# Kernel optimization log

Measured on AMD Instinct MI355X. Metric: run time of the kernel, lower is better.

The kernel has to match this reference:

```python
import jax, jax.numpy as jnp
import numpy as np

B, S, D = 4, 2048, 1024
NEG = -1.0e9


def setup_inputs() -> dict:
    key = jax.random.key(0)
    kq, kk, kv = jax.random.split(key, 3)
    query = jax.random.normal(kq, (B, S, D), dtype=jnp.float32)
    k = jax.random.normal(kk, (B, S, D), dtype=jnp.float32)
    value = jax.random.normal(kv, (B, S, D), dtype=jnp.float32)
    # causal mask: tril(ones(S,S)) with leading broadcast dim, as in the source script
    mask = jnp.tril(jnp.ones((S, S), dtype=jnp.int32))[None, :, :]
    return {"query": query, "key": k, "value": value, "mask": mask}


def reference(query, key, value, mask):
    d_q = query.shape[-1]
    scale = 1.0 / jnp.sqrt(jnp.float32(d_q))
    # [B, S, S] score matrix
    scores = jnp.einsum("bqd,bkd->bqk", query, key) * scale
    scores = jnp.where(mask == 0, jnp.float32(NEG), scores)
    attn = jax.nn.softmax(scores, axis=-1)
    out = jnp.einsum("bqk,bkd->bqd", attn, value)
    return (out, attn)
```

## Files before the change

kernel.cpp:

```cpp
#include <hip/hip_runtime.h>

#define Bn 4
#define Sn 2048
#define Dn 1024

typedef short bf16x8 __attribute__((ext_vector_type(8)));
typedef float f32x4 __attribute__((ext_vector_type(4)));

__device__ __forceinline__ unsigned f2bf(float x) {
    unsigned u = __float_as_uint(x);
    return (u + 0x7FFFu + ((u >> 16) & 1u)) >> 16;
}

__device__ __forceinline__ uint2 pack4(float4 v) {
    uint2 p;
    p.x = f2bf(v.x) | (f2bf(v.y) << 16);
    p.y = f2bf(v.z) | (f2bf(v.w) << 16);
    return p;
}

__device__ __forceinline__ float bf2f(unsigned short s) {
    return __uint_as_float((unsigned)s << 16);
}

__device__ __forceinline__ void gl_lds16(const unsigned short* g, unsigned short* l) {
    __builtin_amdgcn_global_load_lds(
        (const __attribute__((address_space(1))) unsigned int*)g,
        (__attribute__((address_space(3))) unsigned int*)l, 16, 0, 0);
}

__global__ __launch_bounds__(256) void convert_qk_kernel(
    const float* __restrict__ Q, const float* __restrict__ K,
    unsigned short* __restrict__ Q16, unsigned short* __restrict__ K16) {
    size_t i = (size_t)blockIdx.x * 256 + threadIdx.x;
    float4 q = ((const float4*)Q)[i];
    ((uint2*)Q16)[i] = pack4(q);
    float4 k = ((const float4*)K)[i];
    ((uint2*)K16)[i] = pack4(k);
}

__global__ __launch_bounds__(256) void transpose_v_kernel(
    const float* __restrict__ V, unsigned short* __restrict__ Vt) {
    __shared__ unsigned short Ts[128 * 66];
    const int s0 = blockIdx.x * 128, d0 = blockIdx.y * 64, b = blockIdx.z;
    const float* Vb = V + ((size_t)b * Sn + s0) * Dn + d0;
    const int t = threadIdx.x;
#pragma unroll
    for (int i = 0; i < 8; i++) {
        int task = i * 256 + t;
        int r = task >> 4, c4 = task & 15;
        float4 v = *(const float4*)(Vb + (size_t)r * Dn + c4 * 4);
        *(uint2*)(&Ts[r * 66 + c4 * 4]) = pack4(v);
    }
    __syncthreads();
    unsigned short* Vtb = Vt + ((size_t)b * Dn + d0) * Sn + s0;
#pragma unroll
    for (int i = 0; i < 4; i++) {
        int task = i * 256 + t;
        int sc = task & 15, dr = task >> 4;
        unsigned short tmp[8];
#pragma unroll
        for (int j = 0; j < 8; j++) tmp[j] = Ts[(sc * 8 + j) * 66 + dr];
        uint4 u;
        u.x = tmp[0] | ((unsigned)tmp[1] << 16);
        u.y = tmp[2] | ((unsigned)tmp[3] << 16);
        u.z = tmp[4] | ((unsigned)tmp[5] << 16);
        u.w = tmp[6] | ((unsigned)tmp[7] << 16);
        *(uint4*)(&Vtb[(size_t)dr * Sn + sc * 8]) = u;
    }
}

__global__ __launch_bounds__(256) void qk_scores_kernel(
    const unsigned short* __restrict__ Q16, const unsigned short* __restrict__ K16,
    unsigned short* __restrict__ S16) {
    const int wid = blockIdx.x;
    int qt = (int)((sqrtf(8.0f * wid + 1.0f) - 1.0f) * 0.5f);
    while (qt * (qt + 1) / 2 > wid) qt--;
    while ((qt + 1) * (qt + 2) / 2 <= wid) qt++;
    const int kt = wid - qt * (qt + 1) / 2;
    const int b = blockIdx.y;
    __shared__ unsigned short As[2][128 * 64];
    __shared__ unsigned short Bs[2][128 * 64];
    const unsigned short* Ag = Q16 + ((size_t)b * Sn + (size_t)qt * 128) * Dn;
    const unsigned short* Bg = K16 + ((size_t)b * Sn + (size_t)kt * 128) * Dn;
    const int t = threadIdx.x;
    const int w = t >> 6, lane = t & 63;
    const int wm = w >> 1, wn = w & 1;
    const int ml = lane & 15, quad = lane >> 4;
    const int lrow = lane >> 3, lcol = (lane & 7) * 8;
    f32x4 acc[4][4] = {};

    auto stage = [&](int p, int d0) {
#pragma unroll
        for (int j = 0; j < 4; j++) {
            int chunk = w * 4 + j;
            int row = chunk * 8 + lrow;
            gl_lds16(Ag + (size_t)row * Dn + d0 + lcol, &As[p][chunk * 512]);
            gl_lds16(Bg + (size_t)row * Dn + d0 + lcol, &Bs[p][chunk * 512]);
        }
    };

    stage(0, 0);
    int p = 0;
    for (int d0 = 0; d0 < Dn; d0 += 64) {
        __syncthreads();
        if (d0 + 64 < Dn) stage(p ^ 1, d0 + 64);
#pragma unroll
        for (int ko = 0; ko < 2; ko++) {
            bf16x8 af[4], bfr[4];
#pragma unroll
            for (int im = 0; im < 4; im++)
                af[im] = *(const bf16x8*)(&As[p][(wm * 64 + im * 16 + ml) * 64 + ko * 32 + quad * 8]);
#pragma unroll
            for (int in = 0; in < 4; in++)
                bfr[in] = *(const bf16x8*)(&Bs[p][(wn * 64 + in * 16 + ml) * 64 + ko * 32 + quad * 8]);
#pragma unroll
            for (int im = 0; im < 4; im++)
#pragma unroll
                for (int in = 0; in < 4; in++)
                    acc[im][in] = __builtin_amdgcn_mfma_f32_16x16x32_bf16(
                        af[im], bfr[in], acc[im][in], 0, 0, 0);
        }
        p ^= 1;
    }
    unsigned short* outp = S16 + (size_t)b * Sn * Sn + ((size_t)qt * 128) * Sn + kt * 128;
#pragma unroll
    for (int im = 0; im < 4; im++)
#pragma unroll
        for (int in = 0; in < 4; in++)
#pragma unroll
            for (int r = 0; r < 4; r++) {
                int q = wm * 64 + im * 16 + quad * 4 + r;
                int k = wn * 64 + in * 16 + ml;
                outp[(size_t)q * Sn + k] = (unsigned short)f2bf(acc[im][in][r] * 0.03125f);
            }
}

__global__ __launch_bounds__(256) void softmax_kernel(
    unsigned short* __restrict__ SP16, float* __restrict__ attn) {
    const int row = blockIdx.x;
    const int b = row >> 11, q = row & 2047;
    unsigned short* sp = SP16 + (size_t)b * Sn * Sn + (size_t)q * Sn;
    float* ap = attn + (size_t)b * Sn * Sn + (size_t)q * Sn;
    __shared__ float redA[4];
    __shared__ float redB[4];
    const int t = threadIdx.x;
    const int w = t >> 6, lane = t & 63;
    const int nv = q + 1;
    const int nkr = ((q >> 7) + 1) * 128;
    const int base = t * 8;

    float v[8];
    if (base < nv) {
        uint4 u = *(const uint4*)(sp + base);
        v[0] = bf2f((unsigned short)(u.x & 0xFFFF));
        v[1] = bf2f((unsigned short)(u.x >> 16));
        v[2] = bf2f((unsigned short)(u.y & 0xFFFF));
        v[3] = bf2f((unsigned short)(u.y >> 16));
        v[4] = bf2f((unsigned short)(u.z & 0xFFFF));
        v[5] = bf2f((unsigned short)(u.z >> 16));
        v[6] = bf2f((unsigned short)(u.w & 0xFFFF));
        v[7] = bf2f((unsigned short)(u.w >> 16));
#pragma unroll
        for (int j = 0; j < 8; j++)
            if (base + j >= nv) v[j] = -3.0e38f;
    } else {
#pragma unroll
        for (int j = 0; j < 8; j++) v[j] = -3.0e38f;
    }

    float lmax = fmaxf(fmaxf(fmaxf(v[0], v[1]), fmaxf(v[2], v[3])),
                       fmaxf(fmaxf(v[4], v[5]), fmaxf(v[6], v[7])));
#pragma unroll
    for (int o = 32; o > 0; o >>= 1) lmax = fmaxf(lmax, __shfl_xor(lmax, o, 64));
    if (lane == 0) redA[w] = lmax;
    __syncthreads();
    const float m = fmaxf(fmaxf(redA[0], redA[1]), fmaxf(redA[2], redA[3]));

    float lsum = 0.f;
#pragma unroll
    for (int j = 0; j < 8; j++) {
        float e = __expf(v[j] - m);
        v[j] = e;
        lsum += e;
    }
#pragma unroll
    for (int o = 32; o > 0; o >>= 1) lsum += __shfl_xor(lsum, o, 64);
    if (lane == 0) redB[w] = lsum;
    __syncthreads();
    const float inv = 1.0f / (redB[0] + redB[1] + redB[2] + redB[3]);

    float r[8];
#pragma unroll
    for (int j = 0; j < 8; j++) r[j] = v[j] * inv;

    float4 o0 = {r[0], r[1], r[2], r[3]};
    float4 o1 = {r[4], r[5], r[6], r[7]};
    *(float4*)(ap + base) = o0;
    *(float4*)(ap + base + 4) = o1;

    if (base < nkr) {
        uint4 u;
        u.x = f2bf(r[0]) | (f2bf(r[1]) << 16);
        u.y = f2bf(r[2]) | (f2bf(r[3]) << 16);
        u.z = f2bf(r[4]) | (f2bf(r[5]) << 16);
        u.w = f2bf(r[6]) | (f2bf(r[7]) << 16);
        *(uint4*)(sp + base) = u;
    }
}

__global__ __launch_bounds__(256) void pv_kernel(
    const unsigned short* __restrict__ P16, const unsigned short* __restrict__ Vt,
    float* __restrict__ out) {
    const int id = blockIdx.x;
    const int qt = 15 - (id >> 5);
    const int rest = id & 31;
    const int nt = rest & 7, b = rest >> 3;
    __shared__ unsigned short As[2][128 * 64];
    __shared__ unsigned short Bs[2][128 * 64];
    const unsigned short* Ag = P16 + ((size_t)b * Sn + (size_t)qt * 128) * Sn;
    const unsigned short* Bg = Vt + ((size_t)b * Dn + (size_t)nt * 128) * Sn;
    const int t = threadIdx.x;
    const int w = t >> 6, lane = t & 63;
    const int wm = w >> 1, wn = w & 1;
    const int ml = lane & 15, quad = lane >> 4;
    const int lrow = lane >> 3, lcol = (lane & 7) * 8;
    f32x4 acc[4][4] = {};
    const int nk = (qt + 1) * 128;

    auto stage = [&](int p, int k0) {
#pragma unroll
        for (int j = 0; j < 4; j++) {
            int chunk = w * 4 + j;
            int row = chunk * 8 + lrow;
            gl_lds16(Ag + (size_t)row * Sn + k0 + lcol, &As[p][chunk * 512]);
            gl_lds16(Bg + (size_t)row * Sn + k0 + lcol, &Bs[p][chunk * 512]);
        }
    };

    stage(0, 0);
    int p = 0;
    for (int k0 = 0; k0 < nk; k0 += 64) {
        __syncthreads();
        if (k0 + 64 < nk) stage(p ^ 1, k0 + 64);
#pragma unroll
        for (int ko = 0; ko < 2; ko++) {
            bf16x8 af[4], bfr[4];
#pragma unroll
            for (int im = 0; im < 4; im++)
                af[im] = *(const bf16x8*)(&As[p][(wm * 64 + im * 16 + ml) * 64 + ko * 32 + quad * 8]);
#pragma unroll
            for (int in = 0; in < 4; in++)
                bfr[in] = *(const bf16x8*)(&Bs[p][(wn * 64 + in * 16 + ml) * 64 + ko * 32 + quad * 8]);
#pragma unroll
            for (int im = 0; im < 4; im++)
#pragma unroll
                for (int in = 0; in < 4; in++)
                    acc[im][in] = __builtin_amdgcn_mfma_f32_16x16x32_bf16(
                        af[im], bfr[in], acc[im][in], 0, 0, 0);
        }
        p ^= 1;
    }
    float* ob = out + (size_t)b * Sn * Dn + ((size_t)qt * 128) * Dn + nt * 128;
#pragma unroll
    for (int im = 0; im < 4; im++)
#pragma unroll
        for (int in = 0; in < 4; in++)
#pragma unroll
            for (int r = 0; r < 4; r++) {
                int q = wm * 64 + im * 16 + quad * 4 + r;
                int n = wn * 64 + in * 16 + ml;
                ob[(size_t)q * Dn + n] = acc[im][in][r];
            }
}

extern "C" void kernel_launch(void* const* d_in, const int* in_sizes, int n_in,
                              void* d_out, int out_size, void* d_ws, size_t ws_size,
                              hipStream_t stream) {
    const float* Q = (const float*)d_in[0];
    const float* K = (const float*)d_in[1];
    const float* V = (const float*)d_in[2];
    float* out = (float*)d_out;
    float* attn = out + (size_t)Bn * Sn * Dn;

    unsigned short* Q16 = (unsigned short*)d_ws;
    unsigned short* K16 = Q16 + (size_t)Bn * Sn * Dn;
    unsigned short* Vt  = K16 + (size_t)Bn * Sn * Dn;
    unsigned short* SP16 = Vt + (size_t)Bn * Dn * Sn;

    convert_qk_kernel<<<dim3((Bn * Sn * Dn) / (256 * 4)), 256, 0, stream>>>(Q, K, Q16, K16);
    transpose_v_kernel<<<dim3(Sn / 128, Dn / 64, Bn), 256, 0, stream>>>(V, Vt);

    qk_scores_kernel<<<dim3(136, Bn), 256, 0, stream>>>(Q16, K16, SP16);
    softmax_kernel<<<dim3(Bn * Sn), 256, 0, stream>>>(SP16, attn);
    pv_kernel<<<dim3(512), 256, 0, stream>>>(SP16, Vt, out);
}
```

Measured before the change: 289.7 us.

## Swizzle LDS tiles and pipeline A/B staging with split barriers in GEMM kernels

Both the QK and PV GEMM kernels now XOR-swizzle the column slot of each staged row, which avoids LDS bank conflicts on fragment reads. Staging is split: B is prefetched two steps ahead in its own buffer, A one step ahead. Manual vmcnt waits and raw s_barrier calls let global loads overlap the MFMA work. MFMA bursts run at raised wave priority via s_setprio. The risks are that the hand-counted vmcnt(4) waits are fragile and that the B buffer is reused right after the mid-iteration barrier.

```diff
diff --git a/kernel.cpp b/kernel.cpp
--- a/kernel.cpp
+++ b/kernel.cpp
@@ -69,6 +69,7 @@
         *(uint4*)(&Vtb[(size_t)dr * Sn + sc * 8]) = u;
     }
 }
+
 
 __global__ __launch_bounds__(256) void qk_scores_kernel(
     const unsigned short* __restrict__ Q16, const unsigned short* __restrict__ K16,
@@ -87,41 +88,80 @@
     const int w = t >> 6, lane = t & 63;
     const int wm = w >> 1, wn = w & 1;
     const int ml = lane & 15, quad = lane >> 4;
-    const int lrow = lane >> 3, lcol = (lane & 7) * 8;
+    const int srow = lane >> 3, sslot = lane & 7;
     f32x4 acc[4][4] = {};
-
-    auto stage = [&](int p, int d0) {
+    const int NT = Dn / 64;
+
+    auto stageA = [&](int pb, int d0) {
 #pragma unroll
         for (int j = 0; j < 4; j++) {
-            int chunk = w * 4 + j;
-            int row = chunk * 8 + lrow;
-            gl_lds16(Ag + (size_t)row * Dn + d0 + lcol, &As[p][chunk * 512]);
-            gl_lds16(Bg + (size_t)row * Dn + d0 + lcol, &Bs[p][chunk * 512]);
+            int row = w * 32 + j * 8 + srow;
+            int scol = (sslot ^ (row & 7)) * 8;
+            gl_lds16(Ag + (size_t)row * Dn + d0 + scol, &As[pb][(w * 32 + j * 8) * 64]);
         }
     };
-
-    stage(0, 0);
-    int p = 0;
-    for (int d0 = 0; d0 < Dn; d0 += 64) {
-        __syncthreads();
-        if (d0 + 64 < Dn) stage(p ^ 1, d0 + 64);
-#pragma unroll
-        for (int ko = 0; ko < 2; ko++) {
-            bf16x8 af[4], bfr[4];
-#pragma unroll
-            for (int im = 0; im < 4; im++)
-                af[im] = *(const bf16x8*)(&As[p][(wm * 64 + im * 16 + ml) * 64 + ko * 32 + quad * 8]);
-#pragma unroll
-            for (int in = 0; in < 4; in++)
-                bfr[in] = *(const bf16x8*)(&Bs[p][(wn * 64 + in * 16 + ml) * 64 + ko * 32 + quad * 8]);
-#pragma unroll
-            for (int im = 0; im < 4; im++)
-#pragma unroll
-                for (int in = 0; in < 4; in++)
-                    acc[im][in] = __builtin_amdgcn_mfma_f32_16x16x32_bf16(
-                        af[im], bfr[in], acc[im][in], 0, 0, 0);
-        }
-        p ^= 1;
+    auto stageB = [&](int pb, int d0) {
+#pragma unroll
+        for (int j = 0; j < 4; j++) {
+            int row = w * 32 + j * 8 + srow;
+            int scol = (sslot ^ (row & 7)) * 8;
+            gl_lds16(Bg + (size_t)row * Dn + d0 + scol, &Bs[pb][(w * 32 + j * 8) * 64]);
+        }
+    };
+
+    stageA(0, 0);
+    stageB(0, 0);
+    stageB(1, 64);
+    int pb = 0;
+    for (int tau = 0; tau < NT; ++tau) {
+        if (tau == NT - 1) {
+            asm volatile("s_waitcnt vmcnt(0)" ::: "memory");
+        } else {
+            asm volatile("s_waitcnt vmcnt(4)" ::: "memory");
+        }
+        __builtin_amdgcn_s_barrier();
+        asm volatile("" ::: "memory");
+        if (tau + 1 < NT) stageA(pb ^ 1, (tau + 1) * 64);
+        bf16x8 bfr[4][2];
+#pragma unroll
+        for (int in = 0; in < 4; in++)
+#pragma unroll
+            for (int ko = 0; ko < 2; ko++) {
+                int r = wn * 64 + in * 16 + ml;
+                bfr[in][ko] = *(const bf16x8*)(&Bs[pb][r * 64 + ((ko * 4 + quad) ^ (r & 7)) * 8]);
+            }
+        {
+            int r0 = wm * 64 + ml;
+            bf16x8 a0 = *(const bf16x8*)(&As[pb][r0 * 64 + ((quad) ^ (r0 & 7)) * 8]);
+            bf16x8 a1 = *(const bf16x8*)(&As[pb][r0 * 64 + ((4 + quad) ^ (r0 & 7)) * 8]);
+            __builtin_amdgcn_s_setprio(1);
+#pragma unroll
+            for (int in = 0; in < 4; in++)
+                acc[0][in] = __builtin_amdgcn_mfma_f32_16x16x32_bf16(a0, bfr[in][0], acc[0][in], 0, 0, 0);
+#pragma unroll
+            for (int in = 0; in < 4; in++)
+                acc[0][in] = __builtin_amdgcn_mfma_f32_16x16x32_bf16(a1, bfr[in][1], acc[0][in], 0, 0, 0);
+            __builtin_amdgcn_s_setprio(0);
+        }
+        asm volatile("" ::: "memory");
+        __builtin_amdgcn_s_barrier();
+        asm volatile("" ::: "memory");
+        if (tau + 2 < NT) stageB(pb, (tau + 2) * 64);
+#pragma unroll
+        for (int im = 1; im < 4; im++) {
+            int r0 = wm * 64 + im * 16 + ml;
+            bf16x8 a0 = *(const bf16x8*)(&As[pb][r0 * 64 + ((quad) ^ (r0 & 7)) * 8]);
+            bf16x8 a1 = *(const bf16x8*)(&As[pb][r0 * 64 + ((4 + quad) ^ (r0 & 7)) * 8]);
+            __builtin_amdgcn_s_setprio(1);
+#pragma unroll
+            for (int in = 0; in < 4; in++)
+                acc[im][in] = __builtin_amdgcn_mfma_f32_16x16x32_bf16(a0, bfr[in][0], acc[im][in], 0, 0, 0);
+#pragma unroll
+            for (int in = 0; in < 4; in++)
+                acc[im][in] = __builtin_amdgcn_mfma_f32_16x16x32_bf16(a1, bfr[in][1], acc[im][in], 0, 0, 0);
+            __builtin_amdgcn_s_setprio(0);
+        }
+        pb ^= 1;
     }
     unsigned short* outp = S16 + (size_t)b * Sn * Sn + ((size_t)qt * 128) * Sn + kt * 128;
 #pragma unroll
@@ -224,42 +264,80 @@
     const int w = t >> 6, lane = t & 63;
     const int wm = w >> 1, wn = w & 1;
     const int ml = lane & 15, quad = lane >> 4;
-    const int lrow = lane >> 3, lcol = (lane & 7) * 8;
+    const int srow = lane >> 3, sslot = lane & 7;
     f32x4 acc[4][4] = {};
-    const int nk = (qt + 1) * 128;
-
-    auto stage = [&](int p, int k0) {
+    const int NT = (qt + 1) * 2;
+
+    auto stageA = [&](int pb, int k0) {
 #pragma unroll
         for (int j = 0; j < 4; j++) {
-            int chunk = w * 4 + j;
-            int row = chunk * 8 + lrow;
-            gl_lds16(Ag + (size_t)row * Sn + k0 + lcol, &As[p][chunk * 512]);
-            gl_lds16(Bg + (size_t)row * Sn + k0 + lcol, &Bs[p][chunk * 512]);
+            int row = w * 32 + j * 8 + srow;
+            int scol = (sslot ^ (row & 7)) * 8;
+            gl_lds16(Ag + (size_t)row * Sn + k0 + scol, &As[pb][(w * 32 + j * 8) * 64]);
         }
     };
-
-    stage(0, 0);
-    int p = 0;
-    for (int k0 = 0; k0 < nk; k0 += 64) {
-        __syncthreads();
-        if (k0 + 64 < nk) stage(p ^ 1, k0 + 64);
-#pragma unroll
-        for (int ko = 0; ko < 2; ko++) {
-            bf16x8 af[4], bfr[4];
-#pragma unroll
-            for (int im = 0; im < 4; im++)
-                af[im] = *(const bf16x8*)(&As[p][(wm * 64 + im * 16 + ml) * 64 + ko * 32 + quad * 8]);
-#pragma unroll
-            for (int in = 0; in < 4; in++)
-                bfr[in] = *(const bf16x8*)(&Bs[p][(wn * 64 + in * 16 + ml) * 64 + ko * 32 + quad * 8]);
-#pragma unroll
-            for (int im = 0; im < 4; im++)
-#pragma unroll
-                for (int in = 0; in < 4; in++)
-                    acc[im][in] = __builtin_amdgcn_mfma_f32_16x16x32_bf16(
-                        af[im], bfr[in], acc[im][in], 0, 0, 0);
-        }
-        p ^= 1;
+    auto stageB = [&](int pb, int k0) {
+#pragma unroll
+        for (int j = 0; j < 4; j++) {
+            int row = w * 32 + j * 8 + srow;
+            int scol = (sslot ^ (row & 7)) * 8;
+            gl_lds16(Bg + (size_t)row * Sn + k0 + scol, &Bs[pb][(w * 32 + j * 8) * 64]);
+        }
+    };
+
+    stageA(0, 0);
+    stageB(0, 0);
+    stageB(1, 64);
+    int pb = 0;
+    for (int tau = 0; tau < NT; ++tau) {
+        if (tau == NT - 1) {
+            asm volatile("s_waitcnt vmcnt(0)" ::: "memory");
+        } else {
+            asm volatile("s_waitcnt vmcnt(4)" ::: "memory");
+        }
+        __builtin_amdgcn_s_barrier();
+        asm volatile("" ::: "memory");
+        if (tau + 1 < NT) stageA(pb ^ 1, (tau + 1) * 64);
+        bf16x8 bfr[4][2];
+#pragma unroll
+        for (int in = 0; in < 4; in++)
+#pragma unroll
+            for (int ko = 0; ko < 2; ko++) {
+                int r = wn * 64 + in * 16 + ml;
+                bfr[in][ko] = *(const bf16x8*)(&Bs[pb][r * 64 + ((ko * 4 + quad) ^ (r & 7)) * 8]);
+            }
+        {
+            int r0 = wm * 64 + ml;
+            bf16x8 a0 = *(const bf16x8*)(&As[pb][r0 * 64 + ((quad) ^ (r0 & 7)) * 8]);
+            bf16x8 a1 = *(const bf16x8*)(&As[pb][r0 * 64 + ((4 + quad) ^ (r0 & 7)) * 8]);
+            __builtin_amdgcn_s_setprio(1);
+#pragma unroll
+            for (int in = 0; in < 4; in++)
+                acc[0][in] = __builtin_amdgcn_mfma_f32_16x16x32_bf16(a0, bfr[in][0], acc[0][in], 0, 0, 0);
+#pragma unroll
+            for (int in = 0; in < 4; in++)
+                acc[0][in] = __builtin_amdgcn_mfma_f32_16x16x32_bf16(a1, bfr[in][1], acc[0][in], 0, 0, 0);
+            __builtin_amdgcn_s_setprio(0);
+        }
+        asm volatile("" ::: "memory");
+        __builtin_amdgcn_s_barrier();
+        asm volatile("" ::: "memory");
+        if (tau + 2 < NT) stageB(pb, (tau + 2) * 64);
+#pragma unroll
+        for (int im = 1; im < 4; im++) {
+            int r0 = wm * 64 + im * 16 + ml;
+            bf16x8 a0 = *(const bf16x8*)(&As[pb][r0 * 64 + ((quad) ^ (r0 & 7)) * 8]);
+            bf16x8 a1 = *(const bf16x8*)(&As[pb][r0 * 64 + ((4 + quad) ^ (r0 & 7)) * 8]);
+            __builtin_amdgcn_s_setprio(1);
+#pragma unroll
+            for (int in = 0; in < 4; in++)
+                acc[im][in] = __builtin_amdgcn_mfma_f32_16x16x32_bf16(a0, bfr[in][0], acc[im][in], 0, 0, 0);
+#pragma unroll
+            for (int in = 0; in < 4; in++)
+                acc[im][in] = __builtin_amdgcn_mfma_f32_16x16x32_bf16(a1, bfr[in][1], acc[im][in], 0, 0, 0);
+            __builtin_amdgcn_s_setprio(0);
+        }
+        pb ^= 1;
     }
     float* ob = out + (size_t)b * Sn * Dn + ((size_t)qt * 128) * Dn + nt * 128;
 #pragma unroll
```

New measurement: 280.2 us. 1.03x faster.
